# Performance work log

Measured on AMD Instinct MI355X. Metric: run time of the kernel, lower is better.

Reference implementation:

```python
import jax, jax.numpy as jnp
import numpy as np

B, L, H, NH = 8, 200, 128, 4
DH = H // NH
NEG = -2.0**32 + 1.0


def setup_inputs() -> dict:
    key = jax.random.key(0)
    ks = jax.random.split(key, 14)
    f = lambda k, s, sc=1.0: jax.random.normal(k, s, dtype=jnp.float32) * sc
    inp = {
        "queries": f(ks[0], (B, L, H)),
        "keys": f(ks[1], (B, L, H)),
        "time_mask": jax.random.bernoulli(ks[2], 0.1, (B, L)),  # True = padded query row
        "attn_mask": jnp.triu(jnp.ones((L, L), dtype=bool), k=1),  # True = masked (causal)
        "time_matrix_K": f(ks[3], (B, L, L, H), 0.5),
        "time_matrix_V": f(ks[4], (B, L, L, H), 0.5),
        "abs_pos_K": f(ks[5], (B, L, H), 0.5),
        "abs_pos_V": f(ks[6], (B, L, H), 0.5),
        "Qw": f(ks[7], (H, H), H ** -0.5),
        "Qb": f(ks[8], (H,), 0.02),
        "Kw": f(ks[9], (H, H), H ** -0.5),
        "Kb": f(ks[10], (H,), 0.02),
        "Vw": f(ks[11], (H, H), H ** -0.5),
        "Vb": f(ks[12], (H,), 0.02),
    }
    return inp


def reference(queries, keys, time_mask, attn_mask, time_matrix_K, time_matrix_V,
              abs_pos_K, abs_pos_V, Qw, Qb, Kw, Kb, Vw, Vb):
    # Linear projections (torch Linear: x @ W.T + b)
    Q = queries @ Qw.T + Qb                      # [B,L,H]
    K = keys @ Kw.T + Kb
    V = keys @ Vw.T + Vb
    # head split: torch cat(split(.., head_size, dim=-1), dim=0) == contiguous head chunks
    Qh = Q.reshape(B, L, NH, DH)
    Kh = K.reshape(B, L, NH, DH)
    Vh = V.reshape(B, L, NH, DH)
    pKh = abs_pos_K.reshape(B, L, NH, DH)
    pVh = abs_pos_V.reshape(B, L, NH, DH)
    tKh = time_matrix_K.reshape(B, L, L, NH, DH)
    tVh = time_matrix_V.reshape(B, L, L, NH, DH)

    # attention logits: content + absolute-position bias + relative-time bias
    attn = jnp.einsum('blhd,bmhd->bhlm', Qh, Kh)
    attn += jnp.einsum('blhd,bmhd->bhlm', Qh, pKh)
    attn += jnp.einsum('blmhd,blhd->bhlm', tKh, Qh)
    attn = attn / (DH ** 0.5)

    mask = time_mask[:, None, :, None] | attn_mask[None, None, :, :]  # [B,1,L,L] -> broadcast
    attn = jnp.where(mask, NEG, attn)
    attn = jax.nn.softmax(attn, axis=-1)         # [B,NH,L,L]

    out = jnp.einsum('bhlm,bmhd->blhd', attn, Vh)
    out += jnp.einsum('bhlm,bmhd->blhd', attn, pVh)
    out += jnp.einsum('bhlm,blmhd->blhd', attn, tVh)
    return out.reshape(B, L, H)
```

## Files before the change

### kernel.cpp

```cpp
#include <hip/hip_runtime.h>
#include <math.h>

#define B 8
#define L 200
#define H 128
#define NH 4
#define DH 32
#define NEGV (-4294967295.0f)

__global__ __launch_bounds__(128) void proj_kernel(
    const float* __restrict__ queries, const float* __restrict__ keys,
    const float* __restrict__ apK, const float* __restrict__ apV,
    const float* __restrict__ Qw, const float* __restrict__ Qb,
    const float* __restrict__ Kw, const float* __restrict__ Kb,
    const float* __restrict__ Vw, const float* __restrict__ Vb,
    float* __restrict__ Qo, float* __restrict__ Kpo, float* __restrict__ Vpo)
{
    const int j    = threadIdx.x;
    const int row0 = blockIdx.x * 8;

    __shared__ float4 qrow[8 * 32];
    __shared__ float4 krow[8 * 32];

    const float4* q4 = (const float4*)queries + row0 * 32;
    const float4* k4 = (const float4*)keys    + row0 * 32;
    for (int idx = j; idx < 256; idx += 128) { qrow[idx] = q4[idx]; krow[idx] = k4[idx]; }
    __syncthreads();

    float accQ[8], accK[8], accV[8];
    const float qb = Qb[j], kb = Kb[j], vb = Vb[j];
    #pragma unroll
    for (int r = 0; r < 8; ++r) { accQ[r] = qb; accK[r] = kb; accV[r] = vb; }

    const float4* Qw4 = (const float4*)Qw + j * 32;
    const float4* Kw4 = (const float4*)Kw + j * 32;
    const float4* Vw4 = (const float4*)Vw + j * 32;

    for (int k = 0; k < 32; ++k) {
        const float4 wq = Qw4[k];
        const float4 wk = Kw4[k];
        const float4 wv = Vw4[k];
        #pragma unroll
        for (int r = 0; r < 8; ++r) {
            const float4 x = qrow[r * 32 + k];
            accQ[r] = fmaf(wq.x, x.x, fmaf(wq.y, x.y, fmaf(wq.z, x.z, fmaf(wq.w, x.w, accQ[r]))));
            const float4 y = krow[r * 32 + k];
            accK[r] = fmaf(wk.x, y.x, fmaf(wk.y, y.y, fmaf(wk.z, y.z, fmaf(wk.w, y.w, accK[r]))));
            accV[r] = fmaf(wv.x, y.x, fmaf(wv.y, y.y, fmaf(wv.z, y.z, fmaf(wv.w, y.w, accV[r]))));
        }
    }

    #pragma unroll
    for (int r = 0; r < 8; ++r) {
        const int i = row0 + r;
        Qo [i * H + j] = accQ[r];
        Kpo[i * H + j] = accK[r] + apK[i * H + j];
        Vpo[i * H + j] = accV[r] + apV[i * H + j];
    }
}

__global__ __launch_bounds__(512) void attn_kernel(
    const float* __restrict__ Qo, const float* __restrict__ Kp,
    const float* __restrict__ Vp,
    const float* __restrict__ tK, const float* __restrict__ tV,
    const int* __restrict__ tmask, float* __restrict__ out)
{
    const int bid = blockIdx.x;
    const int b   = bid & 7;
    const int l   = 199 - (bid >> 3);
    const int bl  = b * L + l;
    const int t  = threadIdx.x;
    const int c4   = t & 31;
    const int part = t >> 5;
    const int h    = c4 >> 3;

    __shared__ float  S[NH * L];
    __shared__ float4 P[32 * 17];

    const bool rowmasked = (tmask[bl] != 0);
    const float4 q = ((const float4*)Qo)[bl * 32 + c4];

    const float4* Kp4 = (const float4*)Kp + (size_t)b * L * 32;
    const float4* tK4 = (const float4*)tK + (size_t)bl * L * 32;

    if (!rowmasked) {
        const int nsteps = (l + 16) >> 4;
        for (int i0 = 0; i0 < nsteps; i0 += 4) {
            float4 kk[4], tt[4];
            int mm[4];
            #pragma unroll
            for (int u = 0; u < 4; ++u) {
                const int m = part + 16 * (i0 + u);
                mm[u] = m;
                if (m <= l) {
                    kk[u] = Kp4[m * 32 + c4];
                    tt[u] = tK4[m * 32 + c4];
                }
            }
            #pragma unroll
            for (int u = 0; u < 4; ++u) {
                const int m = mm[u];
                float v = 0.0f;
                if (m <= l) {
                    v = fmaf(q.x, kk[u].x + tt[u].x,
                        fmaf(q.y, kk[u].y + tt[u].y,
                        fmaf(q.z, kk[u].z + tt[u].z,
                             q.w * (kk[u].w + tt[u].w))));
                }
                v += __shfl_down(v, 4, 8);
                v += __shfl_down(v, 2, 8);
                v += __shfl_down(v, 1, 8);
                if ((t & 7) == 0 && m <= l)
                    S[h * L + m] = v * 0.17677669529663687f;
            }
        }
    }
    __syncthreads();

    if (!rowmasked && t < 256) {
        const int hw   = t >> 6;
        const int lane = t & 63;
        float mx = -INFINITY;
        for (int m = lane; m <= l; m += 64) mx = fmaxf(mx, S[hw * L + m]);
        #pragma unroll
        for (int off = 32; off; off >>= 1) mx = fmaxf(mx, __shfl_xor(mx, off));
        float s = 0.0f;
        for (int m = lane; m <= l; m += 64) s += __expf(S[hw * L + m] - mx);
        #pragma unroll
        for (int off = 32; off; off >>= 1) s += __shfl_xor(s, off);
        const float inv = 1.0f / s;
        for (int m = lane; m <= l; m += 64)
            S[hw * L + m] = __expf(S[hw * L + m] - mx) * inv;
    }
    __syncthreads();

    const float4* Vp4 = (const float4*)Vp + (size_t)b * L * 32;
    const float4* tV4 = (const float4*)tV + (size_t)bl * L * 32;
    const int   nmV = rowmasked ? L : (l + 1);
    const float wU  = 1.0f / (float)L;
    float4 acc = make_float4(0.f, 0.f, 0.f, 0.f);
    const int nstepsV = (nmV + 15) >> 4;
    for (int i0 = 0; i0 < nstepsV; i0 += 4) {
        float4 vv[4], tt[4];
        int mm[4];
        #pragma unroll
        for (int u = 0; u < 4; ++u) {
            const int m = part + 16 * (i0 + u);
            mm[u] = m;
            if (m < nmV) {
                vv[u] = Vp4[m * 32 + c4];
                tt[u] = tV4[m * 32 + c4];
            }
        }
        #pragma unroll
        for (int u = 0; u < 4; ++u) {
            const int m = mm[u];
            if (m < nmV) {
                const float w = rowmasked ? wU : S[h * L + m];
                acc.x = fmaf(w, vv[u].x + tt[u].x, acc.x);
                acc.y = fmaf(w, vv[u].y + tt[u].y, acc.y);
                acc.z = fmaf(w, vv[u].z + tt[u].z, acc.z);
                acc.w = fmaf(w, vv[u].w + tt[u].w, acc.w);
            }
        }
    }
    P[c4 * 17 + part] = acc;
    __syncthreads();

    if (t < 32) {
        float4 tot = make_float4(0.f, 0.f, 0.f, 0.f);
        #pragma unroll
        for (int p = 0; p < 16; ++p) {
            const float4 a = P[t * 17 + p];
            tot.x += a.x; tot.y += a.y; tot.z += a.z; tot.w += a.w;
        }
        ((float4*)out)[bl * 32 + t] = tot;
    }
}

extern "C" void kernel_launch(void* const* d_in, const int* in_sizes, int n_in,
                              void* d_out, int out_size, void* d_ws, size_t ws_size,
                              hipStream_t stream) {
    const float* queries = (const float*)d_in[0];
    const float* keys    = (const float*)d_in[1];
    const int*   tmask   = (const int*)d_in[2];
    const float* tK   = (const float*)d_in[4];
    const float* tV   = (const float*)d_in[5];
    const float* apK  = (const float*)d_in[6];
    const float* apV  = (const float*)d_in[7];
    const float* Qw   = (const float*)d_in[8];
    const float* Qb   = (const float*)d_in[9];
    const float* Kw   = (const float*)d_in[10];
    const float* Kb   = (const float*)d_in[11];
    const float* Vw   = (const float*)d_in[12];
    const float* Vb   = (const float*)d_in[13];
    float* out = (float*)d_out;

    float* Qo  = (float*)d_ws;
    float* Kpo = Qo  + (size_t)B * L * H;
    float* Vpo = Kpo + (size_t)B * L * H;

    proj_kernel<<<(B * L) / 8, 128, 0, stream>>>(
        queries, keys, apK, apV, Qw, Qb, Kw, Kb, Vw, Vb, Qo, Kpo, Vpo);

    attn_kernel<<<B * L, 512, 0, stream>>>(Qo, Kpo, Vpo, tK, tV, tmask, out);
}
```

Baseline: 346.2 us.

## Pair complementary query rows per block and use nontemporal loads for time matrices

Each attention block now handles two query rows, l and L-1-l, so causal work per block is balanced and the number of blocks is halved. Loads from the large time_matrix_K/V tensors use nontemporal hints to avoid polluting caches with streamed data. The projection loop also gets an unroll-2 pragma. Shared memory per block doubles, and a block now carries twice the register and latency load, which may reduce occupancy.

New measurement: 333.5 us. 3.7% less time.

```diff
diff --git a/kernel.cpp b/kernel.cpp
--- a/kernel.cpp
+++ b/kernel.cpp
@@ -6,7 +6,12 @@
 #define H 128
 #define NH 4
 #define DH 32
-#define NEGV (-4294967295.0f)
+
+typedef float f4v __attribute__((ext_vector_type(4)));
+__device__ __forceinline__ float4 ntld(const float4* p) {
+    f4v v = __builtin_nontemporal_load((const f4v*)p);
+    return make_float4(v[0], v[1], v[2], v[3]);
+}
 
 __global__ __launch_bounds__(128) void proj_kernel(
     const float* __restrict__ queries, const float* __restrict__ keys,
@@ -36,6 +41,7 @@
     const float4* Kw4 = (const float4*)Kw + j * 32;
     const float4* Vw4 = (const float4*)Vw + j * 32;
 
+    #pragma unroll 2
     for (int k = 0; k < 32; ++k) {
         const float4 wq = Qw4[k];
         const float4 wk = Kw4[k];
@@ -59,83 +65,49 @@
     }
 }
 
-__global__ __launch_bounds__(512) void attn_kernel(
-    const float* __restrict__ Qo, const float* __restrict__ Kp,
-    const float* __restrict__ Vp,
-    const float* __restrict__ tK, const float* __restrict__ tV,
-    const int* __restrict__ tmask, float* __restrict__ out)
-{
-    const int bid = blockIdx.x;
-    const int b   = bid & 7;
-    const int l   = 199 - (bid >> 3);
-    const int bl  = b * L + l;
-    const int t  = threadIdx.x;
-    const int c4   = t & 31;
-    const int part = t >> 5;
-    const int h    = c4 >> 3;
-
-    __shared__ float  S[NH * L];
-    __shared__ float4 P[32 * 17];
-
-    const bool rowmasked = (tmask[bl] != 0);
-    const float4 q = ((const float4*)Qo)[bl * 32 + c4];
-
-    const float4* Kp4 = (const float4*)Kp + (size_t)b * L * 32;
-    const float4* tK4 = (const float4*)tK + (size_t)bl * L * 32;
-
-    if (!rowmasked) {
-        const int nsteps = (l + 16) >> 4;
-        for (int i0 = 0; i0 < nsteps; i0 += 4) {
-            float4 kk[4], tt[4];
-            int mm[4];
-            #pragma unroll
-            for (int u = 0; u < 4; ++u) {
-                const int m = part + 16 * (i0 + u);
-                mm[u] = m;
-                if (m <= l) {
-                    kk[u] = Kp4[m * 32 + c4];
-                    tt[u] = tK4[m * 32 + c4];
-                }
-            }
-            #pragma unroll
-            for (int u = 0; u < 4; ++u) {
-                const int m = mm[u];
-                float v = 0.0f;
-                if (m <= l) {
-                    v = fmaf(q.x, kk[u].x + tt[u].x,
-                        fmaf(q.y, kk[u].y + tt[u].y,
-                        fmaf(q.z, kk[u].z + tt[u].z,
-                             q.w * (kk[u].w + tt[u].w))));
-                }
-                v += __shfl_down(v, 4, 8);
-                v += __shfl_down(v, 2, 8);
-                v += __shfl_down(v, 1, 8);
-                if ((t & 7) == 0 && m <= l)
-                    S[h * L + m] = v * 0.17677669529663687f;
-            }
-        }
-    }
-    __syncthreads();
-
-    if (!rowmasked && t < 256) {
-        const int hw   = t >> 6;
-        const int lane = t & 63;
-        float mx = -INFINITY;
-        for (int m = lane; m <= l; m += 64) mx = fmaxf(mx, S[hw * L + m]);
-        #pragma unroll
-        for (int off = 32; off; off >>= 1) mx = fmaxf(mx, __shfl_xor(mx, off));
-        float s = 0.0f;
-        for (int m = lane; m <= l; m += 64) s += __expf(S[hw * L + m] - mx);
-        #pragma unroll
-        for (int off = 32; off; off >>= 1) s += __shfl_xor(s, off);
-        const float inv = 1.0f / s;
-        for (int m = lane; m <= l; m += 64)
-            S[hw * L + m] = __expf(S[hw * L + m] - mx) * inv;
-    }
-    __syncthreads();
-
-    const float4* Vp4 = (const float4*)Vp + (size_t)b * L * 32;
-    const float4* tV4 = (const float4*)tV + (size_t)bl * L * 32;
+
+__device__ __forceinline__ void logits_phase(
+    const float4 q, const int l,
+    const float4* __restrict__ Kp4, const float4* __restrict__ tK4,
+    float* __restrict__ S, const int c4, const int part, const int h)
+{
+    const int nsteps = (l + 16) >> 4;
+    for (int i0 = 0; i0 < nsteps; i0 += 4) {
+        float4 kk[4], tt[4];
+        int mm[4];
+        #pragma unroll
+        for (int u = 0; u < 4; ++u) {
+            const int m = part + 16 * (i0 + u);
+            mm[u] = m;
+            if (m <= l) {
+                kk[u] = Kp4[m * 32 + c4];
+                tt[u] = ntld(&tK4[m * 32 + c4]);
+            }
+        }
+        #pragma unroll
+        for (int u = 0; u < 4; ++u) {
+            const int m = mm[u];
+            float v = 0.0f;
+            if (m <= l) {
+                v = fmaf(q.x, kk[u].x + tt[u].x,
+                    fmaf(q.y, kk[u].y + tt[u].y,
+                    fmaf(q.z, kk[u].z + tt[u].z,
+                         q.w * (kk[u].w + tt[u].w))));
+            }
+            v += __shfl_down(v, 4, 8);
+            v += __shfl_down(v, 2, 8);
+            v += __shfl_down(v, 1, 8);
+            if ((c4 & 7) == 0 && m <= l)
+                S[h * L + m] = v * 0.17677669529663687f;
+        }
+    }
+}
+
+__device__ __forceinline__ float4 pv_phase(
+    const int l, const bool rowmasked,
+    const float4* __restrict__ Vp4, const float4* __restrict__ tV4,
+    const float* __restrict__ S, const int c4, const int part, const int h)
+{
     const int   nmV = rowmasked ? L : (l + 1);
     const float wU  = 1.0f / (float)L;
     float4 acc = make_float4(0.f, 0.f, 0.f, 0.f);
@@ -149,7 +121,7 @@
             mm[u] = m;
             if (m < nmV) {
                 vv[u] = Vp4[m * 32 + c4];
-                tt[u] = tV4[m * 32 + c4];
+                tt[u] = ntld(&tV4[m * 32 + c4]);
             }
         }
         #pragma unroll
@@ -164,17 +136,91 @@
             }
         }
     }
-    P[c4 * 17 + part] = acc;
-    __syncthreads();
-
-    if (t < 32) {
+    return acc;
+}
+
+__global__ __launch_bounds__(512) void attn_kernel(
+    const float* __restrict__ Qo, const float* __restrict__ Kp,
+    const float* __restrict__ Vp,
+    const float* __restrict__ tK, const float* __restrict__ tV,
+    const int* __restrict__ tmask, float* __restrict__ out)
+{
+    const int bid = blockIdx.x;
+    const int b   = bid & 7;
+    const int l1  = bid >> 3;
+    const int l2  = L - 1 - l1;
+    const int bl1 = b * L + l1;
+    const int bl2 = b * L + l2;
+    const int t   = threadIdx.x;
+    const int c4   = t & 31;
+    const int part = t >> 5;
+    const int h    = c4 >> 3;
+
+    __shared__ float  S1[NH * L];
+    __shared__ float  S2[NH * L];
+    __shared__ float4 P1[32 * 17];
+    __shared__ float4 P2[32 * 17];
+
+    const bool rm1 = (tmask[bl1] != 0);
+    const bool rm2 = (tmask[bl2] != 0);
+
+    const float4* Kp4  = (const float4*)Kp + (size_t)b * L * 32;
+    const float4* Vp4  = (const float4*)Vp + (size_t)b * L * 32;
+    const float4* tK41 = (const float4*)tK + (size_t)bl1 * L * 32;
+    const float4* tK42 = (const float4*)tK + (size_t)bl2 * L * 32;
+    const float4* tV41 = (const float4*)tV + (size_t)bl1 * L * 32;
+    const float4* tV42 = (const float4*)tV + (size_t)bl2 * L * 32;
+
+    if (!rm2) {
+        const float4 q2 = ((const float4*)Qo)[bl2 * 32 + c4];
+        logits_phase(q2, l2, Kp4, tK42, S2, c4, part, h);
+    }
+    if (!rm1) {
+        const float4 q1 = ((const float4*)Qo)[bl1 * 32 + c4];
+        logits_phase(q1, l1, Kp4, tK41, S1, c4, part, h);
+    }
+    __syncthreads();
+
+    {
+        const int  half = t >> 8;
+        const int  hw   = (t >> 6) & 3;
+        const int  lane = t & 63;
+        const bool rm   = half ? rm2 : rm1;
+        if (!rm) {
+            const int l  = half ? l2 : l1;
+            float*    Sx = half ? S2 : S1;
+            float mx = -INFINITY;
+            for (int m = lane; m <= l; m += 64) mx = fmaxf(mx, Sx[hw * L + m]);
+            #pragma unroll
+            for (int off = 32; off; off >>= 1) mx = fmaxf(mx, __shfl_xor(mx, off));
+            float s = 0.0f;
+            for (int m = lane; m <= l; m += 64) s += __expf(Sx[hw * L + m] - mx);
+            #pragma unroll
+            for (int off = 32; off; off >>= 1) s += __shfl_xor(s, off);
+            const float inv = 1.0f / s;
+            for (int m = lane; m <= l; m += 64)
+                Sx[hw * L + m] = __expf(Sx[hw * L + m] - mx) * inv;
+        }
+    }
+    __syncthreads();
+
+    const float4 a2 = pv_phase(l2, rm2, Vp4, tV42, S2, c4, part, h);
+    const float4 a1 = pv_phase(l1, rm1, Vp4, tV41, S1, c4, part, h);
+    P1[c4 * 17 + part] = a1;
+    P2[c4 * 17 + part] = a2;
+    __syncthreads();
+
+    if (t < 64) {
+        const int half = t >> 5;
+        const int ch   = t & 31;
+        const float4* Pp = half ? P2 : P1;
         float4 tot = make_float4(0.f, 0.f, 0.f, 0.f);
         #pragma unroll
         for (int p = 0; p < 16; ++p) {
-            const float4 a = P[t * 17 + p];
+            const float4 a = Pp[ch * 17 + p];
             tot.x += a.x; tot.y += a.y; tot.z += a.z; tot.w += a.w;
         }
-        ((float4*)out)[bl * 32 + t] = tot;
+        ((float4*)out)[(half ? bl2 : bl1) * 32 + ch] = tot;
     }
 }
 
@@ -203,5 +249,5 @@
     proj_kernel<<<(B * L) / 8, 128, 0, stream>>>(
         queries, keys, apK, apV, Qw, Qb, Kw, Kb, Vw, Vb, Qo, Kpo, Vpo);
 
-    attn_kernel<<<B * L, 512, 0, stream>>>(Qo, Kpo, Vpo, tK, tV, tmask, out);
-}
+    attn_kernel<<<(B * L) / 2, 512, 0, stream>>>(Qo, Kpo, Vpo, tK, tV, tmask, out);
+}
```
